# Performance work log

Hardware: AMD Instinct MI355X
Metric: run time of the kernel (lower is better)

## Reference

```python
import jax, jax.numpy as jnp
import numpy as np

ITNUM = 100
LAPLACIAN = 0.01
LR = 0.1

_DT0 = jnp.array([[0., 0., 0.], [0., 0., -1.], [0., 1., 0.]], jnp.float32)
_DT1 = jnp.array([[0., 0., 1.], [0., 0., 0.], [-1., 0., 0.]], jnp.float32)
_DT2 = jnp.array([[0., -1., 0.], [1., 0., 0.], [0., 0., 0.]], jnp.float32)


def _rot_and_derivs(angs):
    cx, sx = jnp.cos(angs[0]), jnp.sin(angs[0])
    cy, sy = jnp.cos(angs[1]), jnp.sin(angs[1])
    cz, sz = jnp.cos(angs[2]), jnp.sin(angs[2])
    o = jnp.ones((), angs.dtype)
    z = jnp.zeros((), angs.dtype)
    rotx = jnp.stack([jnp.stack([o, z, z]), jnp.stack([z, cx, -sx]), jnp.stack([z, sx, cx])])
    roty = jnp.stack([jnp.stack([cy, z, sy]), jnp.stack([z, o, z]), jnp.stack([-sy, z, cy])])
    rotz = jnp.stack([jnp.stack([cz, -sz, z]), jnp.stack([sz, cz, z]), jnp.stack([z, z, o])])
    rotxd = jnp.stack([jnp.stack([z, z, z]), jnp.stack([z, -sx, -cx]), jnp.stack([z, cx, -sx])])
    rotyd = jnp.stack([jnp.stack([-sy, z, cy]), jnp.stack([z, z, z]), jnp.stack([-cy, z, -sy])])
    rotzd = jnp.stack([jnp.stack([-sz, -cz, z]), jnp.stack([cz, -sz, z]), jnp.stack([z, z, z])])
    R = rotz @ (roty @ rotx)
    return R, rotz @ roty @ rotxd, rotz @ rotyd @ rotx, rotzd @ roty @ rotx


def _t2T(t):
    z = jnp.zeros((), t.dtype)
    return jnp.stack([
        jnp.stack([z, -t[2], t[1]]),
        jnp.stack([t[2], z, -t[0]]),
        jnp.stack([-t[1], t[0], z]),
    ])


def setup_inputs() -> dict:
    key = jax.random.key(0)
    k1, k2, k3 = jax.random.split(key, 3)
    N = 500000
    H, W = 375.0, 1242.0
    x = jax.random.uniform(k1, (N,), jnp.float32) * (W - 1.0)
    y = jax.random.uniform(k2, (N,), jnp.float32) * (H - 1.0)
    ones = jnp.ones((N,), jnp.float32)
    flow = jax.random.normal(k3, (2, N), jnp.float32) * 3.0  # small optical flow
    pts2d1 = jnp.stack([x, y, ones])                  # [3, N] homogeneous pixels
    pts2d2 = jnp.stack([x + flow[0], y + flow[1], ones])
    intrinsic = jnp.array([[721.5, 0.0, 609.6],
                           [0.0, 721.5, 172.9],
                           [0.0, 0.0, 1.0]], jnp.float32)
    return {"pts2d1": pts2d1, "pts2d2": pts2d2, "intrinsic": intrinsic}


def reference(pts2d1, pts2d2, intrinsic):
    N = pts2d1.shape[1]
    Kinv = jnp.linalg.inv(intrinsic)
    p1 = Kinv @ pts2d1  # normalized coords frame 1, [3, N]
    p2 = Kinv @ pts2d2  # normalized coords frame 2, [3, N]

    def jacobian(ang, t):
        R, rxd, ryd, rzd = _rot_and_derivs(ang)
        T = _t2T(t)
        tn = jnp.linalg.norm(t)
        r_bias = tn - 1.0
        Jt_bias = (2.0 * LAPLACIAN * r_bias / tn) * t  # [3]
        # epipolar residual per point: p2^T (T R) p1
        r = jnp.einsum('in,ij,jn->n', p2, T @ R, p1)
        # six 3x3 derivative matrices: [dE/dang0..2, dE/dt0..2]
        Ms = jnp.stack([T @ rxd, T @ ryd, T @ rzd, _DT0 @ R, _DT1 @ R, _DT2 @ R])
        J = jnp.einsum('in,kij,jn->nk', p2, Ms, p1) * (2.0 * r / N)[:, None]  # [N,6]
        J = J + jnp.concatenate([jnp.zeros((3,), J.dtype), Jt_bias])[None, :] / N
        res = r * r / N + LAPLACIAN * r_bias * r_bias / N  # [N]
        return J, res

    eye6 = jnp.eye(6, dtype=jnp.float32)

    @jax.checkpoint
    def step(carry, _):
        ang, t, min_loss, stopped = carry
        J, res = jacobian(ang, t)
        curloss = jnp.sum(res)
        M = J.T @ J
        Minv = jnp.linalg.inv(M)
        bad_inv = jnp.max(jnp.abs(Minv @ M - eye6)) > 0.1
        stop_now = stopped | bad_inv | (curloss > min_loss)
        update = Minv @ (J.T @ res)  # [6]
        ang_new = jnp.where(stop_now, ang, ang - LR * update[0:3])
        t_new = jnp.where(stop_now, t, t - LR * update[3:6])
        min_new = jnp.where(stop_now, min_loss, curloss)
        return (ang_new, t_new, min_new, stop_now), None

    init = (jnp.zeros((3,), jnp.float32),
            jnp.array([0.0, 0.0, -0.95], jnp.float32),
            jnp.asarray(1e10, jnp.float32),
            jnp.asarray(False))
    (ang, t, _, _), _ = jax.lax.scan(step, init, None, length=ITNUM)

    E_est = _t2T(t / jnp.linalg.norm(t)) @ _rot_and_derivs(ang)[0]
    F_est = Kinv.T @ E_est @ Kinv
    loss_est = jnp.mean(jnp.abs(jnp.einsum('in,ij,jn->n', pts2d2, F_est, pts2d1)))
    return F_est, ang, t, loss_est
```

## Files before the change

### kernel.cpp

```cpp
#include <hip/hip_runtime.h>
#include <math.h>


#define LAPL 0.01
#define LRR  0.1
static constexpr int TS  = 128;
static constexpr int TSP = 129;

__host__ __device__ constexpr int IDXe(int a, int b) { return (a + b) * (a + b + 1) / 2 + b; }

__device__ static const int EA6[6] = {0, 1, 0, 2, 1, 0};
__device__ static const int EB6[6] = {0, 0, 1, 0, 1, 2};
__device__ static const signed char QKt[21] = {0,0,0,0,0,0, 1,1,1,1,1, 2,2,2,2, 3,3,3, 4,4, 5};
__device__ static const signed char QLt[21] = {0,1,2,3,4,5, 1,2,3,4,5, 2,3,4,5, 3,4,5, 4,5, 5};

__device__ __forceinline__ void kinv3d(const float* K, double ki[9]) {
  double a = K[0], b = K[1], c = K[2], d = K[3], e = K[4], f = K[5], g = K[6], h = K[7], i = K[8];
  double A = (e * i - f * h), B = -(d * i - f * g), C = (d * h - e * g);
  double det = a * A + b * B + c * C;
  double r = 1.0 / det;
  ki[0] = A * r;             ki[1] = -(b * i - c * h) * r;  ki[2] =  (b * f - c * e) * r;
  ki[3] = B * r;             ki[4] =  (a * i - c * g) * r;  ki[5] = -(a * f - c * d) * r;
  ki[6] = C * r;             ki[7] = -(a * h - b * g) * r;  ki[8] =  (a * e - b * d) * r;
}

__device__ __forceinline__ void mm3d(const double* A, const double* B, double* C) {
#pragma unroll
  for (int i = 0; i < 3; ++i)
#pragma unroll
    for (int j = 0; j < 3; ++j)
      C[i * 3 + j] = A[i * 3 + 0] * B[0 * 3 + j] + A[i * 3 + 1] * B[1 * 3 + j] + A[i * 3 + 2] * B[2 * 3 + j];
}

__global__ __launch_bounds__(256) void k_zero(double* ws) {
  for (int i = threadIdx.x; i < 1808; i += 256) ws[i] = 0.0;
}

__global__ __launch_bounds__(256) void k_mom(const float* __restrict__ P1, const float* __restrict__ P2f,
                                             const float* __restrict__ K, double* __restrict__ mom, int N) {
  __shared__ double md[2][15][TSP];
  double ki[9];
  kinv3d(K, ki);
  const int t = threadIdx.x;
  const int j2 = t / 15, j1 = t % 15;
  double acc = 0.0;
  for (int base = blockIdx.x * TS; base < N; base += gridDim.x * TS) {
    {
      const int f = t >> 7;
      const int p = t & 127;
      const int idx = base + p;
      double m[15];
      if (idx < N) {
        const float* P = f ? P2f : P1;
        double x = (double)P[idx], y = (double)P[N + idx];
        double u = ki[0] * x + ki[1] * y + ki[2];
        double v = ki[3] * x + ki[4] * y + ki[5];
        double pu[5], pv[5];
        pu[0] = 1.0; pv[0] = 1.0;
        pu[1] = u;  pv[1] = v;
        pu[2] = pu[1] * pu[1]; pv[2] = pv[1] * pv[1];
        pu[3] = pu[2] * pu[1]; pv[3] = pv[2] * pv[1];
        pu[4] = pu[2] * pu[2]; pv[4] = pv[2] * pv[2];
#pragma unroll
        for (int d = 0; d <= 4; ++d)
#pragma unroll
          for (int bb = 0; bb <= d; ++bb)
            m[(d * (d + 1)) / 2 + bb] = pu[d - bb] * pv[bb];
      } else {
#pragma unroll
        for (int q = 0; q < 15; ++q) m[q] = 0.0;
      }
#pragma unroll
      for (int q = 0; q < 15; ++q) md[f][q][p] = m[q];
    }
    __syncthreads();
    if (t < 225) {
#pragma unroll 4
      for (int p = 0; p < TS; ++p) acc += md[1][j2][p] * md[0][j1][p];
    }
    __syncthreads();
  }
  if (t < 225) unsafeAtomicAdd(&mom[(blockIdx.x & 7) * 225 + t], acc);
}

__global__ __launch_bounds__(64) void k_iter(const double* __restrict__ mom, const float* __restrict__ Kg,
                                             float* __restrict__ out, int N) {
  __shared__ struct {
    double Mom[225];
    double G[36 * 37];
    double U0[81];
    double uu[36];
    double gg[36];
    double zd[7][9];
    double Y[7][9];
    double w0[9];
    double Qs[6][6];
    double Cs[6];
    double Ps[6];
    double P2s;
    double Mm[36];
    double vv[6];
    double upd[6];
    double aug[72];
    double sc[6];
    int mul9[81];
    int gcnt[36];
    int gpr[36 * 8];
  } S;
  const int tid = threadIdx.x;
  const double dN = (double)N;
  const double inv2 = 1.0 / (dN * dN);

  for (int i = tid; i < 225; i += 64) {
    double a = 0.0;
#pragma unroll
    for (int c = 0; c < 8; ++c) a += mom[c * 225 + i];
    S.Mom[i] = a;
  }
  for (int i = tid; i < 81; i += 64) {
    int A = i / 9, B = i % 9, ia = A / 3, ja = A % 3, ib = B / 3, jb = B % 3;
    int a2 = (ia == 0) + (ib == 0), b2 = (ia == 1) + (ib == 1);
    int a1 = (ja == 0) + (jb == 0), b1 = (ja == 1) + (jb == 1);
    S.mul9[i] = IDXe(a2, b2) * 6 + IDXe(a1, b1);
  }
  __syncthreads();
  for (int i = tid; i < 1296; i += 64) {
    int ga = i / 36, de = i % 36;
    int g2 = ga / 6, g1 = ga % 6, d2 = de / 6, d1 = de % 6;
    int a2 = EA6[g2] + EA6[d2], b2 = EB6[g2] + EB6[d2];
    int a1 = EA6[g1] + EA6[d1], b1 = EB6[g1] + EB6[d1];
    S.G[ga * 37 + de] = S.Mom[IDXe(a2, b2) * 15 + IDXe(a1, b1)];
  }
  for (int i = tid; i < 81; i += 64) {
    int ga = S.mul9[i];
    S.U0[i] = S.Mom[(ga / 6) * 15 + (ga % 6)];
  }
  if (tid == 0) {
    for (int d = 0; d < 36; ++d) S.gcnt[d] = 0;
    for (int AB = 0; AB < 81; ++AB) {
      int d = S.mul9[AB];
      S.gpr[d * 8 + S.gcnt[d]] = AB;
      S.gcnt[d]++;
    }
  }
  __syncthreads();

  double a0 = 0.0, a1 = 0.0, a2v = 0.0;
  double t0 = 0.0, t1 = 0.0, t2 = -0.95;
  double min_loss = 1e10;

  for (int it = 0; it < 100; ++it) {
    if (tid < 3) {
      double av = (tid == 0) ? a0 : ((tid == 1) ? a1 : a2v);
      double sv, cv;
      sincos(av, &sv, &cv);
      S.sc[tid] = cv;
      S.sc[3 + tid] = sv;
    }
    __syncthreads();
    const double cx = S.sc[0], cy = S.sc[1], cz = S.sc[2];
    const double sx = S.sc[3], sy = S.sc[4], sz = S.sc[5];

    double Rz[9] = {cz, -sz, 0, sz, cz, 0, 0, 0, 1};
    double Ry[9] = {cy, 0, sy, 0, 1, 0, -sy, 0, cy};
    double Rx[9] = {1, 0, 0, 0, cx, -sx, 0, sx, cx};
    double Rzd[9] = {-sz, -cz, 0, cz, -sz, 0, 0, 0, 0};
    double Ryd[9] = {-sy, 0, cy, 0, 0, 0, -cy, 0, -sy};
    double Rxd[9] = {0, 0, 0, 0, -sx, -cx, 0, cx, -sx};
    double YX[9], ZY[9], ZYd[9], ZdY[9], R[9], rxd[9], ryd[9], rzd[9];
    mm3d(Ry, Rx, YX);  mm3d(Rz, YX, R);
    mm3d(Rz, Ry, ZY);  mm3d(ZY, Rxd, rxd);
    mm3d(Rz, Ryd, ZYd); mm3d(ZYd, Rx, ryd);
    mm3d(Rzd, Ry, ZdY); mm3d(ZdY, Rx, rzd);
    double Tm[9] = {0, -t2, t1, t2, 0, -t0, -t1, t0, 0};
    double E[9], M0[9], M1[9], M2[9];
    mm3d(Tm, R, E); mm3d(Tm, rxd, M0); mm3d(Tm, ryd, M1); mm3d(Tm, rzd, M2);
    double M3[9] = {0, 0, 0, -R[6], -R[7], -R[8], R[3], R[4], R[5]};
    double M4[9] = {R[6], R[7], R[8], 0, 0, 0, -R[0], -R[1], -R[2]};
    double M5[9] = {-R[3], -R[4], -R[5], R[0], R[1], R[2], 0, 0, 0};

    if (tid == 0) {
#pragma unroll
      for (int q = 0; q < 9; ++q) {
        S.zd[0][q] = E[q];  S.zd[1][q] = M0[q];
        S.zd[2][q] = M1[q]; S.zd[3][q] = M2[q];
        S.zd[4][q] = M3[q]; S.zd[5][q] = M4[q];
        S.zd[6][q] = M5[q];
      }
    }
    __syncthreads();

    if (tid < 36) {
      double a = 0.0;
      int n = S.gcnt[tid];
      for (int q = 0; q < n; ++q) {
        int ab = S.gpr[tid * 8 + q];
        a += S.zd[0][ab / 9] * S.zd[0][ab % 9];
      }
      S.gg[tid] = a;
    }
    __syncthreads();

    if (tid < 36) {
      double a = 0.0;
#pragma unroll
      for (int q = 0; q < 36; ++q) a += S.G[tid * 37 + q] * S.gg[q];
      S.uu[tid] = a;
    }
    __syncthreads();

    if (tid < 63) {
      int l = tid / 9, A = tid % 9;
      double a = 0.0;
#pragma unroll
      for (int B = 0; B < 9; ++B) a += S.uu[S.mul9[A * 9 + B]] * S.zd[l][B];
      S.Y[l][A] = a;
    }
    __syncthreads();
    if (tid < 9) {
      double a = 0.0;
#pragma unroll
      for (int B = 0; B < 9; ++B) a += S.U0[tid * 9 + B] * S.zd[0][B];
      S.w0[tid] = a;
    }
    __syncthreads();

    if (tid < 21) {
      int k = QKt[tid], l = QLt[tid];
      double a = 0.0;
#pragma unroll
      for (int A = 0; A < 9; ++A) a += S.zd[1 + k][A] * S.Y[1 + l][A];
      S.Qs[k][l] = a; S.Qs[l][k] = a;
    } else if (tid < 27) {
      int k = tid - 21; double a = 0.0;
#pragma unroll
      for (int A = 0; A < 9; ++A) a += S.zd[1 + k][A] * S.Y[0][A];
      S.Cs[k] = a;
    } else if (tid < 33) {
      int k = tid - 27; double a = 0.0;
#pragma unroll
      for (int A = 0; A < 9; ++A) a += S.zd[1 + k][A] * S.w0[A];
      S.Ps[k] = a;
    } else if (tid == 33) {
      double a = 0.0;
#pragma unroll
      for (int A = 0; A < 9; ++A) a += S.zd[0][A] * S.w0[A];
      S.P2s = a;
    }
    __syncthreads();

    double tn = sqrt(t0 * t0 + t1 * t1 + t2 * t2);
    double rbf = tn - 1.0;
    double btc = 2.0 * LAPL * rbf / tn;
    double dcf = (LAPL * rbf * rbf) / dN;
    double curloss = S.P2s / dN + LAPL * rbf * rbf;
#define BVAL(k) ((k) == 3 ? (btc * t0) : (k) == 4 ? (btc * t1) : (k) == 5 ? (btc * t2) : 0.0)
    if (tid < 36) {
      int k = tid / 6, l = tid % 6;
      double bk = BVAL(k), bl = BVAL(l);
      S.Mm[tid] = 4.0 * inv2 * S.Qs[k][l] + 2.0 * inv2 * (bk * S.Ps[l] + bl * S.Ps[k]) + bk * bl / dN;
    } else if (tid < 42) {
      int k = tid - 36;
      double bk = BVAL(k);
      S.vv[k] = 2.0 * inv2 * S.Cs[k] + (2.0 * dcf / dN) * S.Ps[k] + bk * inv2 * S.P2s + bk * dcf;
    }
    __syncthreads();

    for (int e = tid; e < 72; e += 64) {
      int r = e / 12, c = e % 12;
      S.aug[e] = (c < 6) ? S.Mm[r * 6 + c] : ((c - 6 == r) ? 1.0 : 0.0);
    }
    __syncthreads();
    for (int p = 0; p < 6; ++p) {
      double rp = 1.0 / S.aug[p * 12 + p];
      double prc[2], cur[2], mr[2];
      const int ee0 = tid, ee1 = tid + 64;
      { int e = ee0; int r = e / 12, c = e % 12; prc[0] = S.aug[p * 12 + c]; cur[0] = S.aug[e]; mr[0] = S.aug[r * 12 + p]; }
      if (ee1 < 72) { int e = ee1; int r = e / 12, c = e % 12; prc[1] = S.aug[p * 12 + c]; cur[1] = S.aug[e]; mr[1] = S.aug[r * 12 + p]; }
      __syncthreads();
      { int e = ee0; int r = e / 12; S.aug[e] = (r == p) ? prc[0] * rp : cur[0] - mr[0] * rp * prc[0]; }
      if (ee1 < 72) { int e = ee1; int r = e / 12; S.aug[e] = (r == p) ? prc[1] * rp : cur[1] - mr[1] * rp * prc[1]; }
      __syncthreads();
    }

    double merr = 0.0;
    if (tid < 36) {
      int i = tid / 6, j = tid % 6;
      double s2 = -((i == j) ? 1.0 : 0.0);
#pragma unroll
      for (int k2 = 0; k2 < 6; ++k2) s2 += S.aug[i * 12 + 6 + k2] * S.Mm[k2 * 6 + j];
      merr = fabs(s2);
    }
#pragma unroll
    for (int off = 32; off; off >>= 1) merr = fmax(merr, __shfl_xor(merr, off));
    bool bad = merr > 0.1;

    if (tid < 6) {
      double a = 0.0;
#pragma unroll
      for (int j = 0; j < 6; ++j) a += S.aug[tid * 12 + 6 + j] * S.vv[j];
      S.upd[tid] = a;
    }
    __syncthreads();

    bool stop_now = bad || (curloss > min_loss);
    if (stop_now) break;
    a0 -= LRR * S.upd[0]; a1 -= LRR * S.upd[1]; a2v -= LRR * S.upd[2];
    t0 -= LRR * S.upd[3]; t1 -= LRR * S.upd[4]; t2 -= LRR * S.upd[5];
    min_loss = curloss;
    __syncthreads();
  }

  if (tid == 0) {
    double s0, c0, s1, c1, s2, c2;
    sincos(a0, &s0, &c0); sincos(a1, &s1, &c1); sincos(a2v, &s2, &c2);
    double Rz[9] = {c2, -s2, 0, s2, c2, 0, 0, 0, 1};
    double Ry[9] = {c1, 0, s1, 0, 1, 0, -s1, 0, c1};
    double Rx[9] = {1, 0, 0, 0, c0, -s0, 0, s0, c0};
    double YX[9], R[9];
    mm3d(Ry, Rx, YX); mm3d(Rz, YX, R);
    double tn = sqrt(t0 * t0 + t1 * t1 + t2 * t2);
    double n0 = t0 / tn, n1 = t1 / tn, n2 = t2 / tn;
    double Tn[9] = {0, -n2, n1, n2, 0, -n0, -n1, n0, 0};
    double Ee[9];
    mm3d(Tn, R, Ee);
    double ki[9];
    kinv3d(Kg, ki);
    double KT[9] = {ki[0], ki[3], ki[6], ki[1], ki[4], ki[7], ki[2], ki[5], ki[8]};
    double tmp[9], F[9];
    mm3d(KT, Ee, tmp); mm3d(tmp, ki, F);
#pragma unroll
    for (int q = 0; q < 9; ++q) out[q] = (float)F[q];
    out[9] = (float)a0; out[10] = (float)a1; out[11] = (float)a2v;
    out[12] = (float)t0; out[13] = (float)t1; out[14] = (float)t2;
  }
}

__global__ __launch_bounds__(256) void k_loss(const float* __restrict__ P1, const float* __restrict__ P2f,
                                              const float* __restrict__ out, double* __restrict__ lossAcc, int N) {
  const float f0 = out[0], f1 = out[1], f2 = out[2];
  const float f3 = out[3], f4 = out[4], f5 = out[5];
  const float f6 = out[6], f7 = out[7], f8 = out[8];
  double la = 0.0;
  for (int i = blockIdx.x * blockDim.x + threadIdx.x; i < N; i += gridDim.x * blockDim.x) {
    float x1 = P1[i], y1 = P1[N + i], x2 = P2f[i], y2 = P2f[N + i];
    float s = x2 * (f0 * x1 + f1 * y1 + f2) + y2 * (f3 * x1 + f4 * y1 + f5) + (f6 * x1 + f7 * y1 + f8);
    la += (double)fabsf(s);
  }
#pragma unroll
  for (int off = 32; off; off >>= 1) la += __shfl_down(la, off);
  __shared__ double wsum[4];
  int lane = threadIdx.x & 63, w = threadIdx.x >> 6;
  if (lane == 0) wsum[w] = la;
  __syncthreads();
  if (threadIdx.x == 0) {
    double s2 = wsum[0] + wsum[1] + wsum[2] + wsum[3];
    unsafeAtomicAdd(&lossAcc[blockIdx.x & 7], s2);
  }
}

__global__ __launch_bounds__(64) void k_fin(const double* __restrict__ acc, float* __restrict__ out, int N) {
  if (threadIdx.x == 0) {
    double a = 0.0;
#pragma unroll
    for (int c = 0; c < 8; ++c) a += acc[c];
    out[15] = (float)(a / (double)N);
  }
}

extern "C" void kernel_launch(void* const* d_in, const int* in_sizes, int n_in,
                              void* d_out, int out_size, void* d_ws, size_t ws_size,
                              hipStream_t stream) {
  const float* P1 = (const float*)d_in[0];
  const float* P2f = (const float*)d_in[1];
  const float* K = (const float*)d_in[2];
  float* out = (float*)d_out;
  double* ws = (double*)d_ws;
  int N = in_sizes[0] / 3;

  hipLaunchKernelGGL(k_zero, dim3(1), dim3(256), 0, stream, ws);
  hipLaunchKernelGGL(k_mom, dim3(512), dim3(256), 0, stream, P1, P2f, K, ws, N);
  hipLaunchKernelGGL(k_iter, dim3(1), dim3(64), 0, stream, ws, K, out, N);
  hipLaunchKernelGGL(k_loss, dim3(512), dim3(256), 0, stream, P1, P2f, out, ws + 1800, N);
  hipLaunchKernelGGL(k_fin, dim3(1), dim3(64), 0, stream, ws + 1800, out, N);
}
```

Measured before the change: 228.1 us.

## Rework iteration kernel with wave shuffles, register-resident 6x6 inverse, and fused loss finalize

The single-wave iteration kernel now builds the rotation and its derivatives in closed form. It keeps G rows and index tables in registers and inverts the 6x6 system through register shuffles in place of shared-memory Gauss-Jordan, which removes most __syncthreads per iteration. Library sincos and divisions are replaced by a Taylor polynomial and a refined hardware reciprocal. The moment accumulation uses four FMA chains, and the final loss kernel is folded into k_loss with a last-block ticket, dropping one launch. The Taylor sincos is only accurate for small angles, and the pivot-free inverse may behave differently on ill-conditioned matrices.

```diff
diff --git a/kernel.cpp b/kernel.cpp
--- a/kernel.cpp
+++ b/kernel.cpp
@@ -13,17 +13,51 @@
 __device__ static const int EB6[6] = {0, 0, 1, 0, 1, 2};
 __device__ static const signed char QKt[21] = {0,0,0,0,0,0, 1,1,1,1,1, 2,2,2,2, 3,3,3, 4,4, 5};
 __device__ static const signed char QLt[21] = {0,1,2,3,4,5, 1,2,3,4,5, 2,3,4,5, 3,4,5, 4,5, 5};
+
+__device__ __forceinline__ double shfl64(double x, int lane) {
+  int lo = __shfl(__double2loint(x), lane, 64);
+  int hi = __shfl(__double2hiint(x), lane, 64);
+  return __hiloint2double(hi, lo);
+}
+__device__ __forceinline__ double shflx64(double x, int mask) {
+  int lo = __shfl_xor(__double2loint(x), mask, 64);
+  int hi = __shfl_xor(__double2hiint(x), mask, 64);
+  return __hiloint2double(hi, lo);
+}
+__device__ __forceinline__ double fastrcp(double x) {
+  double r = __builtin_amdgcn_rcp(x);
+  double e = fma(-x, r, 1.0); r = fma(r, e, r);
+  e = fma(-x, r, 1.0); r = fma(r, e, r);
+  return r;
+}
+__device__ __forceinline__ void sc_poly(double x, double* s, double* c) {
+  double x2 = x * x;
+  double ss = 1.6059043836821613e-10;
+  ss = fma(ss, x2, -2.5052108385441720e-08);
+  ss = fma(ss, x2, 2.7557319223985893e-06);
+  ss = fma(ss, x2, -1.9841269841269841e-04);
+  ss = fma(ss, x2, 8.3333333333333333e-03);
+  ss = fma(ss, x2, -1.6666666666666666e-01);
+  *s = fma(ss * x2, x, x);
+  double cc = -1.1470745597729725e-11;
+  cc = fma(cc, x2, 2.0876756987868099e-09);
+  cc = fma(cc, x2, -2.7557319223985888e-07);
+  cc = fma(cc, x2, 2.4801587301587302e-05);
+  cc = fma(cc, x2, -1.3888888888888889e-03);
+  cc = fma(cc, x2, 4.1666666666666666e-02);
+  cc = fma(cc, x2, -0.5);
+  *c = fma(cc, x2, 1.0);
+}
 
 __device__ __forceinline__ void kinv3d(const float* K, double ki[9]) {
   double a = K[0], b = K[1], c = K[2], d = K[3], e = K[4], f = K[5], g = K[6], h = K[7], i = K[8];
   double A = (e * i - f * h), B = -(d * i - f * g), C = (d * h - e * g);
   double det = a * A + b * B + c * C;
   double r = 1.0 / det;
-  ki[0] = A * r;             ki[1] = -(b * i - c * h) * r;  ki[2] =  (b * f - c * e) * r;
-  ki[3] = B * r;             ki[4] =  (a * i - c * g) * r;  ki[5] = -(a * f - c * d) * r;
-  ki[6] = C * r;             ki[7] = -(a * h - b * g) * r;  ki[8] =  (a * e - b * d) * r;
-}
-
+  ki[0] = A * r;  ki[1] = -(b * i - c * h) * r;  ki[2] =  (b * f - c * e) * r;
+  ki[3] = B * r;  ki[4] =  (a * i - c * g) * r;  ki[5] = -(a * f - c * d) * r;
+  ki[6] = C * r;  ki[7] = -(a * h - b * g) * r;  ki[8] =  (a * e - b * d) * r;
+}
 __device__ __forceinline__ void mm3d(const double* A, const double* B, double* C) {
 #pragma unroll
   for (int i = 0; i < 3; ++i)
@@ -33,7 +67,7 @@
 }
 
 __global__ __launch_bounds__(256) void k_zero(double* ws) {
-  for (int i = threadIdx.x; i < 1808; i += 256) ws[i] = 0.0;
+  for (int i = threadIdx.x; i < 1812; i += 256) ws[i] = 0.0;
 }
 
 __global__ __launch_bounds__(256) void k_mom(const float* __restrict__ P1, const float* __restrict__ P2f,
@@ -43,7 +77,7 @@
   kinv3d(K, ki);
   const int t = threadIdx.x;
   const int j2 = t / 15, j1 = t % 15;
-  double acc = 0.0;
+  double ac0 = 0.0, ac1 = 0.0, ac2 = 0.0, ac3 = 0.0;
   for (int base = blockIdx.x * TS; base < N; base += gridDim.x * TS) {
     {
       const int f = t >> 7;
@@ -75,12 +109,16 @@
     }
     __syncthreads();
     if (t < 225) {
-#pragma unroll 4
-      for (int p = 0; p < TS; ++p) acc += md[1][j2][p] * md[0][j1][p];
-    }
-    __syncthreads();
-  }
-  if (t < 225) unsafeAtomicAdd(&mom[(blockIdx.x & 7) * 225 + t], acc);
+      for (int p = 0; p < TS; p += 4) {
+        ac0 = fma(md[1][j2][p + 0], md[0][j1][p + 0], ac0);
+        ac1 = fma(md[1][j2][p + 1], md[0][j1][p + 1], ac1);
+        ac2 = fma(md[1][j2][p + 2], md[0][j1][p + 2], ac2);
+        ac3 = fma(md[1][j2][p + 3], md[0][j1][p + 3], ac3);
+      }
+    }
+    __syncthreads();
+  }
+  if (t < 225) unsafeAtomicAdd(&mom[(blockIdx.x & 7) * 225 + t], (ac0 + ac1) + (ac2 + ac3));
 }
 
 __global__ __launch_bounds__(64) void k_iter(const double* __restrict__ mom, const float* __restrict__ Kg,
@@ -89,27 +127,23 @@
     double Mom[225];
     double G[36 * 37];
     double U0[81];
+    double zd[7][9];
+    double gg[36];
+    double w0[9];
     double uu[36];
-    double gg[36];
-    double zd[7][9];
-    double Y[7][9];
-    double w0[9];
-    double Qs[6][6];
-    double Cs[6];
     double Ps[6];
     double P2s;
-    double Mm[36];
-    double vv[6];
-    double upd[6];
-    double aug[72];
-    double sc[6];
+    double Y[63];
+    double Qs[36];
+    double Cs[6];
     int mul9[81];
     int gcnt[36];
-    int gpr[36 * 8];
+    int gpr[36 * 4];
   } S;
   const int tid = threadIdx.x;
   const double dN = (double)N;
-  const double inv2 = 1.0 / (dN * dN);
+  const double invN = 1.0 / dN;
+  const double inv2 = invN * invN;
 
   for (int i = tid; i < 225; i += 64) {
     double a = 0.0;
@@ -139,181 +173,208 @@
     for (int d = 0; d < 36; ++d) S.gcnt[d] = 0;
     for (int AB = 0; AB < 81; ++AB) {
       int d = S.mul9[AB];
-      S.gpr[d * 8 + S.gcnt[d]] = AB;
+      S.gpr[d * 4 + S.gcnt[d]] = AB;
       S.gcnt[d]++;
     }
   }
   __syncthreads();
+
+  double Grow[36];
+  {
+    int gr = (tid < 36) ? tid : 0;
+#pragma unroll
+    for (int q = 0; q < 36; ++q) Grow[q] = S.G[gr * 37 + q];
+  }
+  const int yA = (tid < 63) ? (tid % 9) : 0;
+  const int yl = (tid < 63) ? (tid / 9) : 0;
+  int m9r[9];
+#pragma unroll
+  for (int B = 0; B < 9; ++B) m9r[B] = S.mul9[yA * 9 + B];
+  double u0r[9];
+  {
+    int wA = (tid >= 36 && tid < 45) ? (tid - 36) : 0;
+#pragma unroll
+    for (int B = 0; B < 9; ++B) u0r[B] = S.U0[wA * 9 + B];
+  }
+  int gA[4], gB[4];
+  double gw[4];
+  {
+    int d = (tid < 36) ? tid : 0;
+    int n = S.gcnt[d];
+#pragma unroll
+    for (int q = 0; q < 4; ++q) {
+      int pr = (q < n) ? S.gpr[d * 4 + q] : 0;
+      gA[q] = pr / 9; gB[q] = pr % 9;
+      gw[q] = (q < n) ? 1.0 : 0.0;
+    }
+  }
+  int qk = 0, ql = 0;
+  if (tid < 21) { qk = QKt[tid]; ql = QLt[tid]; }
+  int r6, c6;
+  if (tid < 36)      { r6 = tid / 6;  c6 = tid % 6; }
+  else if (tid < 42) { r6 = tid - 36; c6 = 6; }
+  else               { r6 = 0;        c6 = 0; }
 
   double a0 = 0.0, a1 = 0.0, a2v = 0.0;
   double t0 = 0.0, t1 = 0.0, t2 = -0.95;
   double min_loss = 1e10;
 
+#pragma unroll 1
   for (int it = 0; it < 100; ++it) {
-    if (tid < 3) {
-      double av = (tid == 0) ? a0 : ((tid == 1) ? a1 : a2v);
-      double sv, cv;
-      sincos(av, &sv, &cv);
-      S.sc[tid] = cv;
-      S.sc[3 + tid] = sv;
-    }
-    __syncthreads();
-    const double cx = S.sc[0], cy = S.sc[1], cz = S.sc[2];
-    const double sx = S.sc[3], sy = S.sc[4], sz = S.sc[5];
-
-    double Rz[9] = {cz, -sz, 0, sz, cz, 0, 0, 0, 1};
-    double Ry[9] = {cy, 0, sy, 0, 1, 0, -sy, 0, cy};
-    double Rx[9] = {1, 0, 0, 0, cx, -sx, 0, sx, cx};
-    double Rzd[9] = {-sz, -cz, 0, cz, -sz, 0, 0, 0, 0};
-    double Ryd[9] = {-sy, 0, cy, 0, 0, 0, -cy, 0, -sy};
-    double Rxd[9] = {0, 0, 0, 0, -sx, -cx, 0, cx, -sx};
-    double YX[9], ZY[9], ZYd[9], ZdY[9], R[9], rxd[9], ryd[9], rzd[9];
-    mm3d(Ry, Rx, YX);  mm3d(Rz, YX, R);
-    mm3d(Rz, Ry, ZY);  mm3d(ZY, Rxd, rxd);
-    mm3d(Rz, Ryd, ZYd); mm3d(ZYd, Rx, ryd);
-    mm3d(Rzd, Ry, ZdY); mm3d(ZdY, Rx, rzd);
-    double Tm[9] = {0, -t2, t1, t2, 0, -t0, -t1, t0, 0};
-    double E[9], M0[9], M1[9], M2[9];
-    mm3d(Tm, R, E); mm3d(Tm, rxd, M0); mm3d(Tm, ryd, M1); mm3d(Tm, rzd, M2);
-    double M3[9] = {0, 0, 0, -R[6], -R[7], -R[8], R[3], R[4], R[5]};
-    double M4[9] = {R[6], R[7], R[8], 0, 0, 0, -R[0], -R[1], -R[2]};
-    double M5[9] = {-R[3], -R[4], -R[5], R[0], R[1], R[2], 0, 0, 0};
+    double myang = (tid == 0) ? a0 : (tid == 1) ? a1 : a2v;
+    double ss_, cc_;
+    sc_poly(myang, &ss_, &cc_);
+    const double cx = shfl64(cc_, 0), cy = shfl64(cc_, 1), cz = shfl64(cc_, 2);
+    const double sx = shfl64(ss_, 0), sy = shfl64(ss_, 1), sz = shfl64(ss_, 2);
 
     if (tid == 0) {
-#pragma unroll
-      for (int q = 0; q < 9; ++q) {
-        S.zd[0][q] = E[q];  S.zd[1][q] = M0[q];
-        S.zd[2][q] = M1[q]; S.zd[3][q] = M2[q];
-        S.zd[4][q] = M3[q]; S.zd[5][q] = M4[q];
-        S.zd[6][q] = M5[q];
-      }
+      double czcy = cz * cy, czsy = cz * sy, szcy = sz * cy, szsy = sz * sy;
+      double R0 = czcy;
+      double R1 = czsy * sx - sz * cx;
+      double R2 = czsy * cx + sz * sx;
+      double R3 = szcy;
+      double R4 = szsy * sx + cz * cx;
+      double R5 = szsy * cx - cz * sx;
+      double R6 = -sy;
+      double R7 = cy * sx;
+      double R8 = cy * cx;
+      double y0 = -czsy, y1 = czcy * sx, y2 = czcy * cx;
+      double y3 = -szsy, y4 = szcy * sx, y5 = szcy * cx;
+      double y6 = -cy,   y7 = -(sy * sx), y8 = -(sy * cx);
+      S.zd[0][0] = t1 * R6 - t2 * R3;  S.zd[0][1] = t1 * R7 - t2 * R4;  S.zd[0][2] = t1 * R8 - t2 * R5;
+      S.zd[0][3] = t2 * R0 - t0 * R6;  S.zd[0][4] = t2 * R1 - t0 * R7;  S.zd[0][5] = t2 * R2 - t0 * R8;
+      S.zd[0][6] = t0 * R3 - t1 * R0;  S.zd[0][7] = t0 * R4 - t1 * R1;  S.zd[0][8] = t0 * R5 - t1 * R2;
+      S.zd[1][0] = 0.0;  S.zd[1][1] = t1 * R8 - t2 * R5;  S.zd[1][2] = t2 * R4 - t1 * R7;
+      S.zd[1][3] = 0.0;  S.zd[1][4] = t2 * R2 - t0 * R8;  S.zd[1][5] = t0 * R7 - t2 * R1;
+      S.zd[1][6] = 0.0;  S.zd[1][7] = t0 * R5 - t1 * R2;  S.zd[1][8] = t1 * R1 - t0 * R4;
+      S.zd[2][0] = t1 * y6 - t2 * y3;  S.zd[2][1] = t1 * y7 - t2 * y4;  S.zd[2][2] = t1 * y8 - t2 * y5;
+      S.zd[2][3] = t2 * y0 - t0 * y6;  S.zd[2][4] = t2 * y1 - t0 * y7;  S.zd[2][5] = t2 * y2 - t0 * y8;
+      S.zd[2][6] = t0 * y3 - t1 * y0;  S.zd[2][7] = t0 * y4 - t1 * y1;  S.zd[2][8] = t0 * y5 - t1 * y2;
+      S.zd[3][0] = -t2 * R0;  S.zd[3][1] = -t2 * R1;  S.zd[3][2] = -t2 * R2;
+      S.zd[3][3] = -t2 * R3;  S.zd[3][4] = -t2 * R4;  S.zd[3][5] = -t2 * R5;
+      S.zd[3][6] = t1 * R3 + t0 * R0;  S.zd[3][7] = t1 * R4 + t0 * R1;  S.zd[3][8] = t1 * R5 + t0 * R2;
+      S.zd[4][0] = 0.0; S.zd[4][1] = 0.0; S.zd[4][2] = 0.0;
+      S.zd[4][3] = -R6; S.zd[4][4] = -R7; S.zd[4][5] = -R8;
+      S.zd[4][6] = R3;  S.zd[4][7] = R4;  S.zd[4][8] = R5;
+      S.zd[5][0] = R6;  S.zd[5][1] = R7;  S.zd[5][2] = R8;
+      S.zd[5][3] = 0.0; S.zd[5][4] = 0.0; S.zd[5][5] = 0.0;
+      S.zd[5][6] = -R0; S.zd[5][7] = -R1; S.zd[5][8] = -R2;
+      S.zd[6][0] = -R3; S.zd[6][1] = -R4; S.zd[6][2] = -R5;
+      S.zd[6][3] = R0;  S.zd[6][4] = R1;  S.zd[6][5] = R2;
+      S.zd[6][6] = 0.0; S.zd[6][7] = 0.0; S.zd[6][8] = 0.0;
     }
     __syncthreads();
 
     if (tid < 36) {
-      double a = 0.0;
-      int n = S.gcnt[tid];
-      for (int q = 0; q < n; ++q) {
-        int ab = S.gpr[tid * 8 + q];
-        a += S.zd[0][ab / 9] * S.zd[0][ab % 9];
-      }
-      S.gg[tid] = a;
+      double acc = 0.0;
+#pragma unroll
+      for (int q = 0; q < 4; ++q)
+        acc = fma(gw[q], S.zd[0][gA[q]] * S.zd[0][gB[q]], acc);
+      S.gg[tid] = acc;
+    } else if (tid < 45) {
+      double acc = 0.0;
+#pragma unroll
+      for (int B = 0; B < 9; ++B) acc = fma(u0r[B], S.zd[0][B], acc);
+      S.w0[tid - 36] = acc;
     }
     __syncthreads();
 
     if (tid < 36) {
-      double a = 0.0;
-#pragma unroll
-      for (int q = 0; q < 36; ++q) a += S.G[tid * 37 + q] * S.gg[q];
-      S.uu[tid] = a;
-    }
-    __syncthreads();
-
-    if (tid < 63) {
-      int l = tid / 9, A = tid % 9;
-      double a = 0.0;
-#pragma unroll
-      for (int B = 0; B < 9; ++B) a += S.uu[S.mul9[A * 9 + B]] * S.zd[l][B];
-      S.Y[l][A] = a;
-    }
-    __syncthreads();
-    if (tid < 9) {
-      double a = 0.0;
-#pragma unroll
-      for (int B = 0; B < 9; ++B) a += S.U0[tid * 9 + B] * S.zd[0][B];
-      S.w0[tid] = a;
+      double acc = 0.0;
+#pragma unroll
+      for (int q = 0; q < 36; ++q) acc = fma(Grow[q], S.gg[q], acc);
+      S.uu[tid] = acc;
+    } else if (tid < 43) {
+      int k = tid - 36;
+      int rp = (k < 6) ? (1 + k) : 0;
+      double acc = 0.0;
+#pragma unroll
+      for (int A = 0; A < 9; ++A) acc = fma(S.zd[rp][A], S.w0[A], acc);
+      if (k < 6) S.Ps[k] = acc; else S.P2s = acc;
+    }
+    __syncthreads();
+
+    {
+      double acc = 0.0;
+#pragma unroll
+      for (int B = 0; B < 9; ++B) acc = fma(S.uu[m9r[B]], S.zd[yl][B], acc);
+      if (tid < 63) S.Y[tid] = acc;
     }
     __syncthreads();
 
     if (tid < 21) {
-      int k = QKt[tid], l = QLt[tid];
-      double a = 0.0;
-#pragma unroll
-      for (int A = 0; A < 9; ++A) a += S.zd[1 + k][A] * S.Y[1 + l][A];
-      S.Qs[k][l] = a; S.Qs[l][k] = a;
+      double acc = 0.0;
+#pragma unroll
+      for (int A = 0; A < 9; ++A) acc = fma(S.zd[1 + qk][A], S.Y[(1 + ql) * 9 + A], acc);
+      S.Qs[qk * 6 + ql] = acc;
+      S.Qs[ql * 6 + qk] = acc;
     } else if (tid < 27) {
-      int k = tid - 21; double a = 0.0;
-#pragma unroll
-      for (int A = 0; A < 9; ++A) a += S.zd[1 + k][A] * S.Y[0][A];
-      S.Cs[k] = a;
-    } else if (tid < 33) {
-      int k = tid - 27; double a = 0.0;
-#pragma unroll
-      for (int A = 0; A < 9; ++A) a += S.zd[1 + k][A] * S.w0[A];
-      S.Ps[k] = a;
-    } else if (tid == 33) {
-      double a = 0.0;
-#pragma unroll
-      for (int A = 0; A < 9; ++A) a += S.zd[0][A] * S.w0[A];
-      S.P2s = a;
+      int k = tid - 21;
+      double acc = 0.0;
+#pragma unroll
+      for (int A = 0; A < 9; ++A) acc = fma(S.zd[1 + k][A], S.Y[A], acc);
+      S.Cs[k] = acc;
     }
     __syncthreads();
 
     double tn = sqrt(t0 * t0 + t1 * t1 + t2 * t2);
     double rbf = tn - 1.0;
-    double btc = 2.0 * LAPL * rbf / tn;
-    double dcf = (LAPL * rbf * rbf) / dN;
-    double curloss = S.P2s / dN + LAPL * rbf * rbf;
-#define BVAL(k) ((k) == 3 ? (btc * t0) : (k) == 4 ? (btc * t1) : (k) == 5 ? (btc * t2) : 0.0)
+    double btc = 2.0 * LAPL * rbf * fastrcp(tn);
+    double P2v = S.P2s;
+    double curloss = P2v * invN + LAPL * rbf * rbf;
+    double m = 0.0, mold = 0.0;
     if (tid < 36) {
-      int k = tid / 6, l = tid % 6;
-      double bk = BVAL(k), bl = BVAL(l);
-      S.Mm[tid] = 4.0 * inv2 * S.Qs[k][l] + 2.0 * inv2 * (bk * S.Ps[l] + bl * S.Ps[k]) + bk * bl / dN;
+      int k = r6, l = c6;
+      double bk = (k == 3) ? btc * t0 : (k == 4) ? btc * t1 : (k == 5) ? btc * t2 : 0.0;
+      double bl = (l == 3) ? btc * t0 : (l == 4) ? btc * t1 : (l == 5) ? btc * t2 : 0.0;
+      m = 4.0 * inv2 * S.Qs[tid] + 2.0 * inv2 * (bk * S.Ps[l] + bl * S.Ps[k]) + bk * bl * invN;
+      mold = m;
     } else if (tid < 42) {
-      int k = tid - 36;
-      double bk = BVAL(k);
-      S.vv[k] = 2.0 * inv2 * S.Cs[k] + (2.0 * dcf / dN) * S.Ps[k] + bk * inv2 * S.P2s + bk * dcf;
-    }
-    __syncthreads();
-
-    for (int e = tid; e < 72; e += 64) {
-      int r = e / 12, c = e % 12;
-      S.aug[e] = (c < 6) ? S.Mm[r * 6 + c] : ((c - 6 == r) ? 1.0 : 0.0);
-    }
-    __syncthreads();
+      int k = r6;
+      double bk = (k == 3) ? btc * t0 : (k == 4) ? btc * t1 : (k == 5) ? btc * t2 : 0.0;
+      double dcf = LAPL * rbf * rbf * invN;
+      m = 2.0 * inv2 * S.Cs[k] + (2.0 * dcf * invN) * S.Ps[k] + bk * inv2 * P2v + bk * dcf;
+    }
+
+#pragma unroll
     for (int p = 0; p < 6; ++p) {
-      double rp = 1.0 / S.aug[p * 12 + p];
-      double prc[2], cur[2], mr[2];
-      const int ee0 = tid, ee1 = tid + 64;
-      { int e = ee0; int r = e / 12, c = e % 12; prc[0] = S.aug[p * 12 + c]; cur[0] = S.aug[e]; mr[0] = S.aug[r * 12 + p]; }
-      if (ee1 < 72) { int e = ee1; int r = e / 12, c = e % 12; prc[1] = S.aug[p * 12 + c]; cur[1] = S.aug[e]; mr[1] = S.aug[r * 12 + p]; }
-      __syncthreads();
-      { int e = ee0; int r = e / 12; S.aug[e] = (r == p) ? prc[0] * rp : cur[0] - mr[0] * rp * prc[0]; }
-      if (ee1 < 72) { int e = ee1; int r = e / 12; S.aug[e] = (r == p) ? prc[1] * rp : cur[1] - mr[1] * rp * prc[1]; }
-      __syncthreads();
+      double piv = shfl64(m, p * 7);
+      double d = fastrcp(piv);
+      double prow = shfl64(m, (c6 == 6) ? (36 + p) : (p * 6 + c6));
+      double f = shfl64(m, r6 * 6 + p);
+      double nm = fma(-f, prow * d, m);
+      if (c6 == p) nm = -f * d;
+      if (r6 == p) nm = m * d;
+      if (r6 == p && c6 == p) nm = d;
+      m = nm;
     }
 
     double merr = 0.0;
     if (tid < 36) {
-      int i = tid / 6, j = tid % 6;
-      double s2 = -((i == j) ? 1.0 : 0.0);
-#pragma unroll
-      for (int k2 = 0; k2 < 6; ++k2) s2 += S.aug[i * 12 + 6 + k2] * S.Mm[k2 * 6 + j];
+      double s2 = (r6 == c6) ? -1.0 : 0.0;
+#pragma unroll
+      for (int k = 0; k < 6; ++k)
+        s2 = fma(shfl64(m, r6 * 6 + k), shfl64(mold, k * 6 + c6), s2);
       merr = fabs(s2);
     }
 #pragma unroll
-    for (int off = 32; off; off >>= 1) merr = fmax(merr, __shfl_xor(merr, off));
-    bool bad = merr > 0.1;
-
-    if (tid < 6) {
-      double a = 0.0;
-#pragma unroll
-      for (int j = 0; j < 6; ++j) a += S.aug[tid * 12 + 6 + j] * S.vv[j];
-      S.upd[tid] = a;
-    }
-    __syncthreads();
-
-    bool stop_now = bad || (curloss > min_loss);
+    for (int off = 32; off; off >>= 1) merr = fmax(merr, shflx64(merr, off));
+
+    bool stop_now = (merr > 0.1) || (curloss > min_loss);
     if (stop_now) break;
-    a0 -= LRR * S.upd[0]; a1 -= LRR * S.upd[1]; a2v -= LRR * S.upd[2];
-    t0 -= LRR * S.upd[3]; t1 -= LRR * S.upd[4]; t2 -= LRR * S.upd[5];
+
+    a0  -= LRR * shfl64(m, 36);
+    a1  -= LRR * shfl64(m, 37);
+    a2v -= LRR * shfl64(m, 38);
+    t0  -= LRR * shfl64(m, 39);
+    t1  -= LRR * shfl64(m, 40);
+    t2  -= LRR * shfl64(m, 41);
     min_loss = curloss;
-    __syncthreads();
   }
 
   if (tid == 0) {
     double s0, c0, s1, c1, s2, c2;
-    sincos(a0, &s0, &c0); sincos(a1, &s1, &c1); sincos(a2v, &s2, &c2);
+    sc_poly(a0, &s0, &c0); sc_poly(a1, &s1, &c1); sc_poly(a2v, &s2, &c2);
     double Rz[9] = {c2, -s2, 0, s2, c2, 0, 0, 0, 1};
     double Ry[9] = {c1, 0, s1, 0, 1, 0, -s1, 0, c1};
     double Rx[9] = {1, 0, 0, 0, c0, -s0, 0, s0, c0};
@@ -337,7 +398,9 @@
 }
 
 __global__ __launch_bounds__(256) void k_loss(const float* __restrict__ P1, const float* __restrict__ P2f,
-                                              const float* __restrict__ out, double* __restrict__ lossAcc, int N) {
+                                              float* __restrict__ out, double* __restrict__ ws, int N) {
+  double* lossAcc = ws + 1800;
+  unsigned* ticket = (unsigned*)(ws + 1808);
   const float f0 = out[0], f1 = out[1], f2 = out[2];
   const float f3 = out[3], f4 = out[4], f5 = out[5];
   const float f6 = out[6], f7 = out[7], f8 = out[8];
@@ -356,15 +419,15 @@
   if (threadIdx.x == 0) {
     double s2 = wsum[0] + wsum[1] + wsum[2] + wsum[3];
     unsafeAtomicAdd(&lossAcc[blockIdx.x & 7], s2);
-  }
-}
-
-__global__ __launch_bounds__(64) void k_fin(const double* __restrict__ acc, float* __restrict__ out, int N) {
-  if (threadIdx.x == 0) {
-    double a = 0.0;
-#pragma unroll
-    for (int c = 0; c < 8; ++c) a += acc[c];
-    out[15] = (float)(a / (double)N);
+    __threadfence();
+    unsigned old = atomicAdd(ticket, 1u);
+    if (old == gridDim.x - 1) {
+      __threadfence();
+      double tot = 0.0;
+#pragma unroll
+      for (int c = 0; c < 8; ++c) tot += unsafeAtomicAdd(&lossAcc[c], 0.0);
+      out[15] = (float)(tot / (double)N);
+    }
   }
 }
 
@@ -381,6 +444,5 @@
   hipLaunchKernelGGL(k_zero, dim3(1), dim3(256), 0, stream, ws);
   hipLaunchKernelGGL(k_mom, dim3(512), dim3(256), 0, stream, P1, P2f, K, ws, N);
   hipLaunchKernelGGL(k_iter, dim3(1), dim3(64), 0, stream, ws, K, out, N);
-  hipLaunchKernelGGL(k_loss, dim3(512), dim3(256), 0, stream, P1, P2f, out, ws + 1800, N);
-  hipLaunchKernelGGL(k_fin, dim3(1), dim3(64), 0, stream, ws + 1800, out, N);
-}
+  hipLaunchKernelGGL(k_loss, dim3(512), dim3(256), 0, stream, P1, P2f, out, ws, N);
+}
```

New measurement: 198.4 us. 13.0% less time.
